# Optimization experiments

Hardware: AMD Instinct MI355X
Metric: run time of the kernel (lower is better)

## Reference

```python
import jax, jax.numpy as jnp
import numpy as np

ALPHA = 0.2        # LeakyReLU slope for attention scores (init arg alpha)
MLP_ALPHA = 0.01   # torch nn.LeakyReLU default slope in aftermlp
EPS = 1e-5         # nn.LayerNorm default eps


def leaky(x, a):
    return jnp.where(x >= 0, x, a * x)


def setup_inputs() -> dict:
    key = jax.random.key(0)
    ks = jax.random.split(key, 12)
    B, N, FIN, FOUT, K = 4, 4096, 256, 256, 64
    s = 0.05
    return {
        "h": jax.random.normal(ks[0], (B, N, FIN), jnp.float32),
        "adj": jax.random.uniform(ks[1], (B, N, N), jnp.float32),
        "W": jax.random.normal(ks[2], (FIN, FOUT), jnp.float32) * s,
        "a": jax.random.normal(ks[3], (FOUT, 1), jnp.float32) * s,
        "ln_g": jnp.ones((FOUT,), jnp.float32),
        "ln_b": jnp.zeros((FOUT,), jnp.float32),
        "W1": jax.random.normal(ks[4], (FOUT, FOUT), jnp.float32) * s,
        "b1": jnp.zeros((FOUT,), jnp.float32),
        "W2": jax.random.normal(ks[5], (FOUT, FOUT), jnp.float32) * s,
        "b2": jnp.zeros((FOUT,), jnp.float32),
        "W3": jax.random.normal(ks[6], (FOUT, FOUT), jnp.float32) * s,
        "b3": jnp.zeros((FOUT,), jnp.float32),
        "k": K,
    }


def reference(h, adj, W, a, ln_g, ln_b, W1, b1, W2, b2, W3, b3, k):
    # Wh: [B, N, F]
    Wh = h @ W
    B, N, Fd = Wh.shape
    C = N // k
    Whc = Wh.reshape(B, C, k, Fd)                       # [B, C, k, F]
    # a_input[b,c,i,j] = Wh[b,c,i]  =>  e[b,c,i,j] = leaky(Wh[b,c,i] . a)
    e = leaky(jnp.squeeze(Whc @ a, -1), ALPHA)          # [B, C, k]
    # block-diagonal chunks of adj: [B, C, k, k]
    idx = jnp.arange(C)
    blocks = adj.reshape(B, C, k, C, k)[:, idx, :, idx, :]  # [C, B, k, k]
    blocks = jnp.transpose(blocks, (1, 0, 2, 3))            # [B, C, k, k]
    scores = jax.nn.softmax(blocks * e[..., :, None], axis=-1)  # [B, C, k, k]
    out = jnp.einsum('bcij,bcjf->bcif', scores, Whc)    # [B, C, k, F]
    # aftermlp: Linear -> LeakyReLU(0.01) -> Linear -> LeakyReLU(0.01) -> Linear
    y = leaky(out @ W1 + b1, MLP_ALPHA)
    y = leaky(y @ W2 + b2, MLP_ALPHA)
    y = y @ W3 + b3
    # residual + LayerNorm over last dim
    z = y + out
    mu = jnp.mean(z, axis=-1, keepdims=True)
    var = jnp.var(z, axis=-1, keepdims=True)
    z = (z - mu) / jnp.sqrt(var + EPS) * ln_g + ln_b
    return z.reshape(B, N, Fd)
```

## Files before the change

kernel.cpp:

```cpp
#include <hip/hip_runtime.h>

typedef __bf16 bf16;
typedef __bf16 bf16x4 __attribute__((ext_vector_type(4)));
typedef __bf16 bf16x8 __attribute__((ext_vector_type(8)));
typedef float  f32x4  __attribute__((ext_vector_type(4)));

#define ALPHA 0.2f
#define MLP_ALPHA 0.01f
#define LN_EPS 1e-5f

constexpr int Bb = 4;
constexpr int Nn = 4096;
constexpr int Ff = 256;
constexpr int Kk = 64;
constexpr int Cc = 64;

__device__ __forceinline__ f32x4 MFMA(bf16x8 a, bf16x8 b, f32x4 c) {
  return __builtin_amdgcn_mfma_f32_16x16x32_bf16(a, b, c, 0, 0, 0);
}
__device__ __forceinline__ bf16x4 pack4(f32x4 v) {
  bf16x4 r; r[0]=(bf16)v[0]; r[1]=(bf16)v[1]; r[2]=(bf16)v[2]; r[3]=(bf16)v[3]; return r;
}
__device__ __forceinline__ int swz512(int i, int inrow) { return i*512 + (inrow ^ ((i & 15) << 4)); }
__device__ __forceinline__ int swz128(int f, int inrow) { return f*128 + (inrow ^ ((f & 7) << 4)); }

__global__ __launch_bounds__(256) void prep_weights(
    const float* __restrict__ W0, const float* __restrict__ W1,
    const float* __restrict__ W2, const float* __restrict__ W3,
    const float* __restrict__ a_vec,
    bf16* __restrict__ outw, float* __restrict__ wa)
{
  if (blockIdx.x == 128) {
    int k = threadIdx.x;
    const float* row = W0 + k * Ff;
    float s = 0.f;
    for (int j = 0; j < Ff; j += 4) {
      f32x4 wv = *(const f32x4*)(row + j);
      f32x4 av = *(const f32x4*)(a_vec + j);
      s += wv[0]*av[0] + wv[1]*av[1] + wv[2]*av[2] + wv[3]*av[3];
    }
    wa[k] = s;
    return;
  }
  int t = blockIdx.x * 256 + threadIdx.x;
  int l = t & 63, nt = (t >> 6) & 15, kt = (t >> 10) & 7, mat = t >> 13;
  const float* src = (mat==0) ? W0 : (mat==1) ? W1 : (mat==2) ? W2 : W3;
  int n  = nt*16 + (l & 15);
  int k0 = kt*32 + (l >> 4)*8;
  bf16x8 v;
  #pragma unroll
  for (int jj = 0; jj < 8; ++jj) v[jj] = (bf16)src[(k0 + jj)*Ff + n];
  *(bf16x8*)(outw + (size_t)t * 8) = v;
}

__global__ __launch_bounds__(512, 2) void gat_mfma(
    const float* __restrict__ h,   const float* __restrict__ adj,
    const float* __restrict__ gln, const float* __restrict__ bln,
    const float* __restrict__ b1,  const float* __restrict__ b2,
    const float* __restrict__ b3,
    const bf16* __restrict__ wfrag, const float* __restrict__ wa,
    float* __restrict__ out)
{
  __shared__ bf16 hbs[Kk * Ff];
  __shared__ bf16 bufA[Ff * Kk];
  __shared__ bf16 bufB[Kk * Ff];
  __shared__ bf16 sShi[Kk * Kk];
  __shared__ bf16 sSlo[Kk * Kk];
  __shared__ float evec[Kk];
  __shared__ float lnS[Kk * 8], lnQ[Kk * 8];

  const int t = threadIdx.x, l = t & 63, w = t >> 6, g = l >> 4, li = l & 15;
  const int bc = blockIdx.x, b = bc >> 6, c = bc & 63;
  const size_t rbase = (size_t)b * Nn + c * Kk;

  float adjv[8];
  #pragma unroll
  for (int rr = 0; rr < 8; ++rr)
    adjv[rr] = adj[(rbase + w*8 + rr) * Nn + (size_t)c*Kk + l];

  {
    const int i  = t >> 3;
    const int k0 = (t & 7) * 32;
    const float* hp = h + (rbase + i) * Ff + k0;
    float p = 0.f;
    #pragma unroll
    for (int u = 0; u < 4; ++u) {
      f32x4 h0 = *(const f32x4*)(hp + u*8);
      f32x4 h1 = *(const f32x4*)(hp + u*8 + 4);
      f32x4 w0 = *(const f32x4*)(wa + k0 + u*8);
      f32x4 w1 = *(const f32x4*)(wa + k0 + u*8 + 4);
      p += h0[0]*w0[0] + h0[1]*w0[1] + h0[2]*w0[2] + h0[3]*w0[3]
         + h1[0]*w1[0] + h1[1]*w1[1] + h1[2]*w1[2] + h1[3]*w1[3];
      bf16x8 v;
      #pragma unroll
      for (int d = 0; d < 4; ++d) { v[d] = (bf16)h0[d]; v[4+d] = (bf16)h1[d]; }
      *(bf16x8*)((char*)hbs + swz512(i, (k0 + u*8)*2)) = v;
    }
    p += __shfl_xor(p, 1); p += __shfl_xor(p, 2); p += __shfl_xor(p, 4);
    if ((l & 7) == 0) evec[i] = (p >= 0.f) ? p : ALPHA * p;
  }
  __syncthreads();

  #pragma unroll
  for (int rr = 0; rr < 8; ++rr) {
    int i = w*8 + rr;
    float x = adjv[rr] * evec[i];
    float m = x;
    #pragma unroll
    for (int off = 32; off; off >>= 1) m = fmaxf(m, __shfl_xor(m, off));
    float pe = __expf(x - m);
    float s = pe;
    #pragma unroll
    for (int off = 32; off; off >>= 1) s += __shfl_xor(s, off);
    float sv = pe / s;
    bf16 hi = (bf16)sv;
    *(bf16*)((char*)sShi + swz128(i, l*2)) = hi;
    *(bf16*)((char*)sSlo + swz128(i, l*2)) = (bf16)(sv - (float)hi);
  }

  f32x4 acc1[2][4];
  #pragma unroll
  for (int q = 0; q < 2; ++q)
    #pragma unroll
    for (int rt = 0; rt < 4; ++rt) acc1[q][rt] = (f32x4){0.f,0.f,0.f,0.f};
  #pragma unroll
  for (int kt = 0; kt < 8; ++kt) {
    bf16x8 af[4];
    #pragma unroll
    for (int rt = 0; rt < 4; ++rt) {
      int i = rt*16 + li;
      af[rt] = *(const bf16x8*)((const char*)hbs + swz512(i, (kt*32 + g*8)*2));
    }
    #pragma unroll
    for (int q = 0; q < 2; ++q) {
      bf16x8 bfr = *(const bf16x8*)(wfrag + (((size_t)kt*16 + (w*2 + q))*64 + l)*8);
      #pragma unroll
      for (int rt = 0; rt < 4; ++rt) acc1[q][rt] = MFMA(af[rt], bfr, acc1[q][rt]);
    }
  }
  #pragma unroll
  for (int q = 0; q < 2; ++q) {
    int f = (w*2 + q)*16 + li;
    #pragma unroll
    for (int rt = 0; rt < 4; ++rt) {
      int j0 = rt*16 + g*4;
      *(bf16x4*)((char*)bufA + swz128(f, j0*2)) = pack4(acc1[q][rt]);
    }
  }
  __syncthreads();

  f32x4 xr[4][2];
  #pragma unroll
  for (int nt = 0; nt < 4; ++nt)
    #pragma unroll
    for (int r = 0; r < 2; ++r) xr[nt][r] = (f32x4){0.f,0.f,0.f,0.f};
  #pragma unroll
  for (int kt = 0; kt < 2; ++kt) {
    int koff = (kt*32 + g*8)*2;
    bf16x8 af[2], bfrH[4], bfrL[4];
    #pragma unroll
    for (int r = 0; r < 2; ++r) {
      int f = (w*2 + r)*16 + li;
      af[r] = *(const bf16x8*)((const char*)bufA + swz128(f, koff));
    }
    #pragma unroll
    for (int nt = 0; nt < 4; ++nt) {
      int i = nt*16 + li;
      bfrH[nt] = *(const bf16x8*)((const char*)sShi + swz128(i, koff));
      bfrL[nt] = *(const bf16x8*)((const char*)sSlo + swz128(i, koff));
    }
    #pragma unroll
    for (int nt = 0; nt < 4; ++nt)
      #pragma unroll
      for (int r = 0; r < 2; ++r) {
        xr[nt][r] = MFMA(af[r], bfrL[nt], xr[nt][r]);
        xr[nt][r] = MFMA(af[r], bfrH[nt], xr[nt][r]);
      }
  }
  #pragma unroll
  for (int nt = 0; nt < 4; ++nt) {
    int i = nt*16 + li;
    #pragma unroll
    for (int r = 0; r < 2; ++r) {
      int f0 = (w*2 + r)*16 + g*4;
      *(bf16x4*)((char*)bufB + swz512(i, f0*2)) = pack4(xr[nt][r]);
    }
  }
  __syncthreads();

  f32x4 acc3[4][2];
  #pragma unroll
  for (int stage = 0; stage < 3; ++stage) {
    const bf16* inB = (stage == 1) ? bufA : bufB;
    #pragma unroll
    for (int nt = 0; nt < 4; ++nt)
      #pragma unroll
      for (int r = 0; r < 2; ++r) acc3[nt][r] = (f32x4){0.f,0.f,0.f,0.f};
    #pragma unroll
    for (int kt = 0; kt < 8; ++kt) {
      bf16x8 af[2], bfr[4];
      #pragma unroll
      for (int r = 0; r < 2; ++r)
        af[r] = *(const bf16x8*)(wfrag + ((((size_t)(stage+1)*8 + kt)*16 + (w*2 + r))*64 + l)*8);
      #pragma unroll
      for (int nt = 0; nt < 4; ++nt) {
        int i = nt*16 + li;
        bfr[nt] = *(const bf16x8*)((const char*)inB + swz512(i, (kt*32 + g*8)*2));
      }
      #pragma unroll
      for (int nt = 0; nt < 4; ++nt)
        #pragma unroll
        for (int r = 0; r < 2; ++r)
          acc3[nt][r] = MFMA(af[r], bfr[nt], acc3[nt][r]);
    }
    if (stage == 2) break;
    __syncthreads();
    const float* bias = (stage == 0) ? b1 : b2;
    bf16* outB = (stage == 0) ? bufA : bufB;
    #pragma unroll
    for (int nt = 0; nt < 4; ++nt) {
      int i = nt*16 + li;
      #pragma unroll
      for (int r = 0; r < 2; ++r) {
        f32x4 v;
        #pragma unroll
        for (int e = 0; e < 4; ++e) {
          float x = acc3[nt][r][e] + bias[(w*2 + r)*16 + g*4 + e];
          v[e] = (x >= 0.f) ? x : MLP_ALPHA * x;
        }
        int f0 = (w*2 + r)*16 + g*4;
        *(bf16x4*)((char*)outB + swz512(i, f0*2)) = pack4(v);
      }
    }
    __syncthreads();
  }

  {
    float bv[2][4], gv[2][4], btv[2][4];
    #pragma unroll
    for (int r = 0; r < 2; ++r)
      #pragma unroll
      for (int e = 0; e < 4; ++e) {
        int f = (w*2 + r)*16 + g*4 + e;
        bv[r][e] = b3[f]; gv[r][e] = gln[f]; btv[r][e] = bln[f];
      }
    #pragma unroll
    for (int nt = 0; nt < 4; ++nt) {
      float s = 0.f, qq = 0.f;
      #pragma unroll
      for (int r = 0; r < 2; ++r)
        #pragma unroll
        for (int e = 0; e < 4; ++e) {
          float z = acc3[nt][r][e] + bv[r][e] + xr[nt][r][e];
          acc3[nt][r][e] = z;
          s += z; qq += z*z;
        }
      s  += __shfl_xor(s, 16);  s  += __shfl_xor(s, 32);
      qq += __shfl_xor(qq, 16); qq += __shfl_xor(qq, 32);
      if (g == 0) {
        int i = nt*16 + li;
        lnS[i*8 + w] = s;
        lnQ[i*8 + w] = qq;
      }
    }
    __syncthreads();
    #pragma unroll
    for (int nt = 0; nt < 4; ++nt) {
      int i = nt*16 + li;
      f32x4 s0 = *(const f32x4*)&lnS[i*8];
      f32x4 s1 = *(const f32x4*)&lnS[i*8 + 4];
      f32x4 q0 = *(const f32x4*)&lnQ[i*8];
      f32x4 q1 = *(const f32x4*)&lnQ[i*8 + 4];
      float s  = s0[0]+s0[1]+s0[2]+s0[3]+s1[0]+s1[1]+s1[2]+s1[3];
      float qq = q0[0]+q0[1]+q0[2]+q0[3]+q1[0]+q1[1]+q1[2]+q1[3];
      float mu  = s * (1.f/256.f);
      float var = qq * (1.f/256.f) - mu*mu;
      float rs  = rsqrtf(var + LN_EPS);
      #pragma unroll
      for (int r = 0; r < 2; ++r) {
        float4 o;
        o.x = (acc3[nt][r][0] - mu)*rs*gv[r][0] + btv[r][0];
        o.y = (acc3[nt][r][1] - mu)*rs*gv[r][1] + btv[r][1];
        o.z = (acc3[nt][r][2] - mu)*rs*gv[r][2] + btv[r][2];
        o.w = (acc3[nt][r][3] - mu)*rs*gv[r][3] + btv[r][3];
        *(float4*)&out[(rbase + i)*Ff + (w*2 + r)*16 + g*4] = o;
      }
    }
  }
}

extern "C" void kernel_launch(void* const* d_in, const int* in_sizes, int n_in,
                              void* d_out, int out_size, void* d_ws, size_t ws_size,
                              hipStream_t stream) {
  (void)in_sizes; (void)n_in; (void)out_size; (void)ws_size;
  bf16*  wfrag = (bf16*)d_ws;
  float* wa    = (float*)((char*)d_ws + 512*1024);
  prep_weights<<<dim3(129), dim3(256), 0, stream>>>(
      (const float*)d_in[2], (const float*)d_in[6],
      (const float*)d_in[8], (const float*)d_in[10],
      (const float*)d_in[3], wfrag, wa);
  gat_mfma<<<dim3(Bb * Cc), dim3(512), 0, stream>>>(
      (const float*)d_in[0],  (const float*)d_in[1],
      (const float*)d_in[4],  (const float*)d_in[5],
      (const float*)d_in[7],  (const float*)d_in[9],  (const float*)d_in[11],
      wfrag, wa, (float*)d_out);
}
```

Measured before the change: 38.31 us.

## Double threads per block, splitting row tiles across two wave groups

Raises the block from 512 to 1024 threads (16 waves). The extra waves split the 64 rows of each chunk into two halves (wi), while the 8-wave feature split (wf) stays the same. Per-wave accumulators and MFMA work are halved, which gives more latency hiding and less register pressure per wave. The costs are more redundant weight-fragment loads from global memory (each B fragment is now loaded by two waves), heavier barriers, and launch_bounds(1024,4) forcing a tighter register budget.

Result: faster. 36.07 us (-5.8%).

```diff
diff --git a/kernel.cpp b/kernel.cpp
--- a/kernel.cpp
+++ b/kernel.cpp
@@ -53,7 +53,7 @@
   *(bf16x8*)(outw + (size_t)t * 8) = v;
 }
 
-__global__ __launch_bounds__(512, 2) void gat_mfma(
+__global__ __launch_bounds__(1024, 4) void gat_mfma(
     const float* __restrict__ h,   const float* __restrict__ adj,
     const float* __restrict__ gln, const float* __restrict__ bln,
     const float* __restrict__ b1,  const float* __restrict__ b2,
@@ -70,21 +70,23 @@
   __shared__ float lnS[Kk * 8], lnQ[Kk * 8];
 
   const int t = threadIdx.x, l = t & 63, w = t >> 6, g = l >> 4, li = l & 15;
+  const int wf = w & 7;
+  const int wi = w >> 3;
   const int bc = blockIdx.x, b = bc >> 6, c = bc & 63;
   const size_t rbase = (size_t)b * Nn + c * Kk;
 
-  float adjv[8];
-  #pragma unroll
-  for (int rr = 0; rr < 8; ++rr)
-    adjv[rr] = adj[(rbase + w*8 + rr) * Nn + (size_t)c*Kk + l];
+  float adjv[4];
+  #pragma unroll
+  for (int rr = 0; rr < 4; ++rr)
+    adjv[rr] = adj[(rbase + w*4 + rr) * Nn + (size_t)c*Kk + l];
 
   {
-    const int i  = t >> 3;
-    const int k0 = (t & 7) * 32;
+    const int i  = t >> 4;
+    const int k0 = (t & 15) * 16;
     const float* hp = h + (rbase + i) * Ff + k0;
     float p = 0.f;
     #pragma unroll
-    for (int u = 0; u < 4; ++u) {
+    for (int u = 0; u < 2; ++u) {
       f32x4 h0 = *(const f32x4*)(hp + u*8);
       f32x4 h1 = *(const f32x4*)(hp + u*8 + 4);
       f32x4 w0 = *(const f32x4*)(wa + k0 + u*8);
@@ -96,14 +98,15 @@
       for (int d = 0; d < 4; ++d) { v[d] = (bf16)h0[d]; v[4+d] = (bf16)h1[d]; }
       *(bf16x8*)((char*)hbs + swz512(i, (k0 + u*8)*2)) = v;
     }
-    p += __shfl_xor(p, 1); p += __shfl_xor(p, 2); p += __shfl_xor(p, 4);
-    if ((l & 7) == 0) evec[i] = (p >= 0.f) ? p : ALPHA * p;
+    p += __shfl_xor(p, 1); p += __shfl_xor(p, 2);
+    p += __shfl_xor(p, 4); p += __shfl_xor(p, 8);
+    if ((t & 15) == 0) evec[i] = (p >= 0.f) ? p : ALPHA * p;
   }
   __syncthreads();
 
   #pragma unroll
-  for (int rr = 0; rr < 8; ++rr) {
-    int i = w*8 + rr;
+  for (int rr = 0; rr < 4; ++rr) {
+    int i = w*4 + rr;
     float x = adjv[rr] * evec[i];
     float m = x;
     #pragma unroll
@@ -118,59 +121,59 @@
     *(bf16*)((char*)sSlo + swz128(i, l*2)) = (bf16)(sv - (float)hi);
   }
 
-  f32x4 acc1[2][4];
+  f32x4 acc1[2][2];
   #pragma unroll
   for (int q = 0; q < 2; ++q)
     #pragma unroll
-    for (int rt = 0; rt < 4; ++rt) acc1[q][rt] = (f32x4){0.f,0.f,0.f,0.f};
+    for (int rt = 0; rt < 2; ++rt) acc1[q][rt] = (f32x4){0.f,0.f,0.f,0.f};
   #pragma unroll
   for (int kt = 0; kt < 8; ++kt) {
-    bf16x8 af[4];
-    #pragma unroll
-    for (int rt = 0; rt < 4; ++rt) {
-      int i = rt*16 + li;
+    bf16x8 af[2];
+    #pragma unroll
+    for (int rt = 0; rt < 2; ++rt) {
+      int i = (wi*2 + rt)*16 + li;
       af[rt] = *(const bf16x8*)((const char*)hbs + swz512(i, (kt*32 + g*8)*2));
     }
     #pragma unroll
     for (int q = 0; q < 2; ++q) {
-      bf16x8 bfr = *(const bf16x8*)(wfrag + (((size_t)kt*16 + (w*2 + q))*64 + l)*8);
-      #pragma unroll
-      for (int rt = 0; rt < 4; ++rt) acc1[q][rt] = MFMA(af[rt], bfr, acc1[q][rt]);
+      bf16x8 bfr = *(const bf16x8*)(wfrag + (((size_t)kt*16 + (wf*2 + q))*64 + l)*8);
+      #pragma unroll
+      for (int rt = 0; rt < 2; ++rt) acc1[q][rt] = MFMA(af[rt], bfr, acc1[q][rt]);
     }
   }
   #pragma unroll
   for (int q = 0; q < 2; ++q) {
-    int f = (w*2 + q)*16 + li;
-    #pragma unroll
-    for (int rt = 0; rt < 4; ++rt) {
-      int j0 = rt*16 + g*4;
+    int f = (wf*2 + q)*16 + li;
+    #pragma unroll
+    for (int rt = 0; rt < 2; ++rt) {
+      int j0 = (wi*2 + rt)*16 + g*4;
       *(bf16x4*)((char*)bufA + swz128(f, j0*2)) = pack4(acc1[q][rt]);
     }
   }
   __syncthreads();
 
-  f32x4 xr[4][2];
-  #pragma unroll
-  for (int nt = 0; nt < 4; ++nt)
+  f32x4 xr[2][2];
+  #pragma unroll
+  for (int nt = 0; nt < 2; ++nt)
     #pragma unroll
     for (int r = 0; r < 2; ++r) xr[nt][r] = (f32x4){0.f,0.f,0.f,0.f};
   #pragma unroll
   for (int kt = 0; kt < 2; ++kt) {
     int koff = (kt*32 + g*8)*2;
-    bf16x8 af[2], bfrH[4], bfrL[4];
+    bf16x8 af[2], bfrH[2], bfrL[2];
     #pragma unroll
     for (int r = 0; r < 2; ++r) {
-      int f = (w*2 + r)*16 + li;
+      int f = (wf*2 + r)*16 + li;
       af[r] = *(const bf16x8*)((const char*)bufA + swz128(f, koff));
     }
     #pragma unroll
-    for (int nt = 0; nt < 4; ++nt) {
-      int i = nt*16 + li;
+    for (int nt = 0; nt < 2; ++nt) {
+      int i = (wi*2 + nt)*16 + li;
       bfrH[nt] = *(const bf16x8*)((const char*)sShi + swz128(i, koff));
       bfrL[nt] = *(const bf16x8*)((const char*)sSlo + swz128(i, koff));
     }
     #pragma unroll
-    for (int nt = 0; nt < 4; ++nt)
+    for (int nt = 0; nt < 2; ++nt)
       #pragma unroll
       for (int r = 0; r < 2; ++r) {
         xr[nt][r] = MFMA(af[r], bfrL[nt], xr[nt][r]);
@@ -178,37 +181,37 @@
       }
   }
   #pragma unroll
-  for (int nt = 0; nt < 4; ++nt) {
-    int i = nt*16 + li;
+  for (int nt = 0; nt < 2; ++nt) {
+    int i = (wi*2 + nt)*16 + li;
     #pragma unroll
     for (int r = 0; r < 2; ++r) {
-      int f0 = (w*2 + r)*16 + g*4;
+      int f0 = (wf*2 + r)*16 + g*4;
       *(bf16x4*)((char*)bufB + swz512(i, f0*2)) = pack4(xr[nt][r]);
     }
   }
   __syncthreads();
 
-  f32x4 acc3[4][2];
+  f32x4 acc3[2][2];
   #pragma unroll
   for (int stage = 0; stage < 3; ++stage) {
     const bf16* inB = (stage == 1) ? bufA : bufB;
     #pragma unroll
-    for (int nt = 0; nt < 4; ++nt)
+    for (int nt = 0; nt < 2; ++nt)
       #pragma unroll
       for (int r = 0; r < 2; ++r) acc3[nt][r] = (f32x4){0.f,0.f,0.f,0.f};
     #pragma unroll
     for (int kt = 0; kt < 8; ++kt) {
-      bf16x8 af[2], bfr[4];
+      bf16x8 af[2], bfr[2];
       #pragma unroll
       for (int r = 0; r < 2; ++r)
-        af[r] = *(const bf16x8*)(wfrag + ((((size_t)(stage+1)*8 + kt)*16 + (w*2 + r))*64 + l)*8);
-      #pragma unroll
-      for (int nt = 0; nt < 4; ++nt) {
-        int i = nt*16 + li;
+        af[r] = *(const bf16x8*)(wfrag + ((((size_t)(stage+1)*8 + kt)*16 + (wf*2 + r))*64 + l)*8);
+      #pragma unroll
+      for (int nt = 0; nt < 2; ++nt) {
+        int i = (wi*2 + nt)*16 + li;
         bfr[nt] = *(const bf16x8*)((const char*)inB + swz512(i, (kt*32 + g*8)*2));
       }
       #pragma unroll
-      for (int nt = 0; nt < 4; ++nt)
+      for (int nt = 0; nt < 2; ++nt)
         #pragma unroll
         for (int r = 0; r < 2; ++r)
           acc3[nt][r] = MFMA(af[r], bfr[nt], acc3[nt][r]);
@@ -218,17 +221,17 @@
     const float* bias = (stage == 0) ? b1 : b2;
     bf16* outB = (stage == 0) ? bufA : bufB;
     #pragma unroll
-    for (int nt = 0; nt < 4; ++nt) {
-      int i = nt*16 + li;
+    for (int nt = 0; nt < 2; ++nt) {
+      int i = (wi*2 + nt)*16 + li;
       #pragma unroll
       for (int r = 0; r < 2; ++r) {
         f32x4 v;
         #pragma unroll
         for (int e = 0; e < 4; ++e) {
-          float x = acc3[nt][r][e] + bias[(w*2 + r)*16 + g*4 + e];
+          float x = acc3[nt][r][e] + bias[(wf*2 + r)*16 + g*4 + e];
           v[e] = (x >= 0.f) ? x : MLP_ALPHA * x;
         }
-        int f0 = (w*2 + r)*16 + g*4;
+        int f0 = (wf*2 + r)*16 + g*4;
         *(bf16x4*)((char*)outB + swz512(i, f0*2)) = pack4(v);
       }
     }
@@ -241,11 +244,11 @@
     for (int r = 0; r < 2; ++r)
       #pragma unroll
       for (int e = 0; e < 4; ++e) {
-        int f = (w*2 + r)*16 + g*4 + e;
+        int f = (wf*2 + r)*16 + g*4 + e;
         bv[r][e] = b3[f]; gv[r][e] = gln[f]; btv[r][e] = bln[f];
       }
     #pragma unroll
-    for (int nt = 0; nt < 4; ++nt) {
+    for (int nt = 0; nt < 2; ++nt) {
       float s = 0.f, qq = 0.f;
       #pragma unroll
       for (int r = 0; r < 2; ++r)
@@ -258,15 +261,15 @@
       s  += __shfl_xor(s, 16);  s  += __shfl_xor(s, 32);
       qq += __shfl_xor(qq, 16); qq += __shfl_xor(qq, 32);
       if (g == 0) {
-        int i = nt*16 + li;
-        lnS[i*8 + w] = s;
-        lnQ[i*8 + w] = qq;
+        int i = (wi*2 + nt)*16 + li;
+        lnS[i*8 + wf] = s;
+        lnQ[i*8 + wf] = qq;
       }
     }
     __syncthreads();
     #pragma unroll
-    for (int nt = 0; nt < 4; ++nt) {
-      int i = nt*16 + li;
+    for (int nt = 0; nt < 2; ++nt) {
+      int i = (wi*2 + nt)*16 + li;
       f32x4 s0 = *(const f32x4*)&lnS[i*8];
       f32x4 s1 = *(const f32x4*)&lnS[i*8 + 4];
       f32x4 q0 = *(const f32x4*)&lnQ[i*8];
@@ -283,7 +286,7 @@
         o.y = (acc3[nt][r][1] - mu)*rs*gv[r][1] + btv[r][1];
         o.z = (acc3[nt][r][2] - mu)*rs*gv[r][2] + btv[r][2];
         o.w = (acc3[nt][r][3] - mu)*rs*gv[r][3] + btv[r][3];
-        *(float4*)&out[(rbase + i)*Ff + (w*2 + r)*16 + g*4] = o;
+        *(float4*)&out[(rbase + i)*Ff + (wf*2 + r)*16 + g*4] = o;
       }
     }
   }
@@ -299,7 +302,7 @@
       (const float*)d_in[2], (const float*)d_in[6],
       (const float*)d_in[8], (const float*)d_in[10],
       (const float*)d_in[3], wfrag, wa);
-  gat_mfma<<<dim3(Bb * Cc), dim3(512), 0, stream>>>(
+  gat_mfma<<<dim3(Bb * Cc), dim3(1024), 0, stream>>>(
       (const float*)d_in[0],  (const float*)d_in[1],
       (const float*)d_in[4],  (const float*)d_in[5],
       (const float*)d_in[7],  (const float*)d_in[9],  (const float*)d_in[11],
```
